# Kernel tuning notes

Measured on AMD Instinct MI355X. Metric: run time of the kernel, lower is better.

## Reference

```python
import jax, jax.numpy as jnp
import numpy as np

NUM_HEADS = 32
HEAD_DIM = 128
NUM_KV_HEADS = 8
SCALE = 0.08838834764831845  # 1/sqrt(128)
T = 2048          # total packed tokens (total_q == total_k in delta branch)
N_SAL = 512       # number of salient rows
NUM_SEQS = 4
EPS = 1e-8
NEG = -1e30


def setup_inputs() -> dict:
    key = jax.random.key(0)
    ks = jax.random.split(key, 5)
    q = jax.random.normal(ks[0], (T, NUM_HEADS, HEAD_DIM), dtype=jnp.float32)
    k = jax.random.normal(ks[1], (T, NUM_KV_HEADS, HEAD_DIM), dtype=jnp.float32)
    v = jax.random.normal(ks[2], (N_SAL, NUM_KV_HEADS, HEAD_DIM), dtype=jnp.float32)
    v_cache = jax.random.normal(ks[3], (T, NUM_KV_HEADS, HEAD_DIM), dtype=jnp.float32)
    c_cache = jax.random.normal(ks[4], (T, NUM_HEADS * HEAD_DIM), dtype=jnp.float32)
    # unique, sorted salient row indices (torch index_copy requires well-defined scatter)
    idx_salient_row = (jnp.arange(N_SAL, dtype=jnp.int64) * (T // N_SAL))
    # 4 equal packed sequences
    cu_seqlens = jnp.array([0, 512, 1024, 1536, 2048], dtype=jnp.int64)
    return {"q": q, "k": k, "v": v, "v_cache": v_cache, "c_cache": c_cache,
            "idx_salient_row": idx_salient_row, "cu_seqlens": cu_seqlens}


def _segment_ids(cu_seqlens, n):
    # seg[i] = which packed sequence row i belongs to (searchsorted right on bounds)
    return jnp.searchsorted(cu_seqlens[1:], jnp.arange(n), side="right")


def _sdpa(q_, k_, v_, seg_q_, seg_k_):
    # GQA: repeat_interleave kv heads to match query heads
    n_rep = q_.shape[1] // k_.shape[1]
    if n_rep > 1:
        k_ = jnp.repeat(k_, n_rep, axis=1)
        v_ = jnp.repeat(v_, n_rep, axis=1)
    scores = jnp.einsum("qhd,khd->hqk", q_, k_) * SCALE  # [H, nq, T]
    allow = (seg_q_[:, None] == seg_k_[None, :])          # [nq, T]
    scores = jnp.where(allow[None, :, :], scores, NEG)
    p = jax.nn.softmax(scores, axis=-1)
    return jnp.einsum("hqk,khd->qhd", p, v_)              # [nq, H, D]


def reference(q, k, v, v_cache, c_cache, idx_salient_row, cu_seqlens):
    total = q.shape[0]
    seg = _segment_ids(cu_seqlens, total)  # seg_q == seg_k (total_q == total_k)

    # delta KV-cache update at salient rows
    v_delta = v - v_cache[idx_salient_row]                      # [n_sal, Hkv, D]
    v_delta_sparse = jnp.zeros_like(k).at[idx_salient_row].set(v_delta)
    v_cache_new = v_cache.at[idx_salient_row].set(v)

    # salient-row full attention against updated cache
    o_salient = _sdpa(q[idx_salient_row], k, v_cache_new, seg[idx_salient_row], seg)
    # sparse delta attention for every row
    delta_c = _sdpa(q, k, v_delta_sparse, seg, seg)

    new_c_flat = c_cache + delta_c.reshape(total, -1)
    new_c_flat = new_c_flat.at[idx_salient_row].set(o_salient.reshape(o_salient.shape[0], -1))

    # cosine similarity between old and new context (early-exit signal)
    num = jnp.sum(c_cache * new_c_flat, axis=-1)
    den_c = jnp.sum(c_cache * c_cache, axis=-1)
    den_n = jnp.sum(new_c_flat * new_c_flat, axis=-1)
    cos_sim = num / (jnp.sqrt(den_c) * jnp.sqrt(den_n) + EPS)

    return new_c_flat.reshape(total, NUM_HEADS, HEAD_DIM), cos_sim
```

## Files before the change

kernel.cpp:

```cpp
#include <hip/hip_runtime.h>
#include <math.h>

#define NUM_HEADS 32
#define HEAD_DIM 128
#define NUM_KV_HEADS 8
#define SCALE 0.08838834764831845f
#define EPS 1e-8f
#define MAX_SEG 512
#define QT 32
#define BLK 512
#define SEGC_MAX 16
#define PB_STRIDE 520
#define TLD 130
#define CD (NUM_HEADS * HEAD_DIM)

typedef __bf16 bf16x8 __attribute__((ext_vector_type(8)));
typedef __bf16 bf16x4 __attribute__((ext_vector_type(4)));
typedef float  f32x4  __attribute__((ext_vector_type(4)));

__device__ __forceinline__ int lower_bound_i(const int* __restrict__ a, int n, int key) {
    int lo = 0, hi = n;
    while (lo < hi) { int mid = (lo + hi) >> 1; if (a[mid] < key) lo = mid + 1; else hi = mid; }
    return lo;
}
__device__ __forceinline__ int bsearch_eq(const int* __restrict__ a, int n, int key) {
    int lo = lower_bound_i(a, n, key);
    return (lo < n && a[lo] == key) ? lo : -1;
}

__device__ __forceinline__ bf16x8 cvt8(const float* p) {
    float4 f0 = *(const float4*)p;
    float4 f1 = *(const float4*)(p + 4);
    bf16x8 a;
    a[0]=(__bf16)f0.x; a[1]=(__bf16)f0.y; a[2]=(__bf16)f0.z; a[3]=(__bf16)f0.w;
    a[4]=(__bf16)f1.x; a[5]=(__bf16)f1.y; a[6]=(__bf16)f1.z; a[7]=(__bf16)f1.w;
    return a;
}

__device__ __forceinline__ void red16(float& xn, float& xc, float& xd) {
#pragma unroll
    for (int m = 1; m <= 8; m <<= 1) {
        xn += __shfl_xor(xn, m, 64);
        xc += __shfl_xor(xc, m, 64);
        xd += __shfl_xor(xd, m, 64);
    }
}

__global__ void prep(const float* __restrict__ k, const float* __restrict__ v,
                     const float* __restrict__ vc, const int* __restrict__ idx,
                     const int* __restrict__ cu,
                     __bf16* __restrict__ kb, __bf16* __restrict__ vnewT,
                     __bf16* __restrict__ vdScat, int* __restrict__ tinfo,
                     int* __restrict__ rowsal,
                     int T, int Tpad, int n_sal, int n_seq,
                     int nb_conv, int nb_vt) {
    __shared__ __bf16 tileN[64 * TLD];
    __shared__ __bf16 tileD[64 * TLD];
    __shared__ int sal_of[64];
    const int b = blockIdx.x;
    const int tid = threadIdx.x;

    if (b < nb_conv) {
        int i = b * 256 + tid;
        int n8 = T * NUM_KV_HEADS * HEAD_DIM / 8;
        if (i < n8) {
            const float4* s4 = (const float4*)(k + (size_t)i * 8);
            float4 a = s4[0], bb = s4[1];
            bf16x8 o;
            o[0]=(__bf16)a.x; o[1]=(__bf16)a.y; o[2]=(__bf16)a.z; o[3]=(__bf16)a.w;
            o[4]=(__bf16)bb.x; o[5]=(__bf16)bb.y; o[6]=(__bf16)bb.z; o[7]=(__bf16)bb.w;
            *(bf16x8*)(kb + (size_t)i * 8) = o;
        }
        return;
    }
    if (b < nb_conv + nb_vt * NUM_KV_HEADS) {
        const int bb = b - nb_conv;
        const int kv = bb / nb_vt;
        const int r0 = (bb % nb_vt) * 64;
        if (tid < 64) sal_of[tid] = bsearch_eq(idx, n_sal, r0 + tid);
        __syncthreads();
        for (int ii = tid; ii < 64 * 32; ii += 256) {
            int r = ii >> 5, c4 = ii & 31;
            int row = r0 + r;
            float4 fN = {0.f, 0.f, 0.f, 0.f};
            float4 fD = {0.f, 0.f, 0.f, 0.f};
            if (row < T) {
                int s2 = sal_of[r];
                if (s2 >= 0) {
                    float4 a  = *(const float4*)(v  + ((size_t)s2  * NUM_KV_HEADS + kv) * HEAD_DIM + c4 * 4);
                    float4 c  = *(const float4*)(vc + ((size_t)row * NUM_KV_HEADS + kv) * HEAD_DIM + c4 * 4);
                    fN = a;
                    fD.x = a.x - c.x; fD.y = a.y - c.y; fD.z = a.z - c.z; fD.w = a.w - c.w;
                } else {
                    fN = *(const float4*)(vc + ((size_t)row * NUM_KV_HEADS + kv) * HEAD_DIM + c4 * 4);
                }
            }
            __bf16* tn = &tileN[r * TLD + c4 * 4];
            tn[0] = (__bf16)fN.x; tn[1] = (__bf16)fN.y; tn[2] = (__bf16)fN.z; tn[3] = (__bf16)fN.w;
            __bf16* td = &tileD[r * TLD + c4 * 4];
            td[0] = (__bf16)fD.x; td[1] = (__bf16)fD.y; td[2] = (__bf16)fD.z; td[3] = (__bf16)fD.w;
        }
        __syncthreads();
        for (int ii = tid; ii < 128 * 8; ii += 256) {
            int d = ii >> 3, rg = ii & 7;
            int row_out = r0 + rg * 8;
            if (row_out < Tpad) {
                bf16x8 oN, oD;
#pragma unroll
                for (int j = 0; j < 8; j++) {
                    oN[j] = tileN[(rg * 8 + j) * TLD + d];
                    oD[j] = tileD[(rg * 8 + j) * TLD + d];
                }
                *(bf16x8*)(vnewT  + ((size_t)kv * HEAD_DIM + d) * Tpad + row_out) = oN;
                *(bf16x8*)(vdScat + ((size_t)kv * HEAD_DIM + d) * Tpad + row_out) = oD;
            }
        }
        return;
    }
    {
        for (int i = tid; i < T; i += 256) rowsal[i] = -1;
        __syncthreads();
        for (int s = tid; s < n_sal; s += 256) rowsal[idx[s]] = s;
        const int NT = T / QT;
        for (int t = tid; t < NT; t += 256) {
            const int r0 = t * QT;
            int a = 0, e = T;
            for (int s = 0; s < n_seq; s++) {
                int x = cu[s], y = cu[s + 1];
                if (r0 >= x && r0 < y) { a = x; e = y; }
            }
            tinfo[t * 4 + 0] = a;
            tinfo[t * 4 + 1] = e;
            tinfo[t * 4 + 2] = 0;
            tinfo[t * 4 + 3] = 0;
        }
    }
}


#define QK_TILE(ttc, FULLSEG) {                                                             \
    const int t_ = wave * 4 + (ttc);                                                        \
    if ((FULLSEG) || t_ < ntiles) {                                                         \
        int key_ = seg_start + t_ * 16 + lm;                                                \
        if (!(FULLSEG) && key_ >= seg_end) key_ = seg_end - 1;                              \
        const __bf16* kp_ = kb + ((size_t)key_ * NUM_KV_HEADS + kvh) * HEAD_DIM + quad * 8; \
        const bf16x8 bk0_ = *(const bf16x8*)(kp_);                                          \
        const bf16x8 bk1_ = *(const bf16x8*)(kp_ + 32);                                     \
        const bf16x8 bk2_ = *(const bf16x8*)(kp_ + 64);                                     \
        const bf16x8 bk3_ = *(const bf16x8*)(kp_ + 96);                                     \
        f32x4 a0_ = {0.f,0.f,0.f,0.f}, a1_ = {0.f,0.f,0.f,0.f};                             \
        a0_ = __builtin_amdgcn_mfma_f32_16x16x32_bf16(bk0_, aq00, a0_, 0, 0, 0);            \
        a1_ = __builtin_amdgcn_mfma_f32_16x16x32_bf16(bk0_, aq10, a1_, 0, 0, 0);            \
        a0_ = __builtin_amdgcn_mfma_f32_16x16x32_bf16(bk1_, aq01, a0_, 0, 0, 0);            \
        a1_ = __builtin_amdgcn_mfma_f32_16x16x32_bf16(bk1_, aq11, a1_, 0, 0, 0);            \
        a0_ = __builtin_amdgcn_mfma_f32_16x16x32_bf16(bk2_, aq02, a0_, 0, 0, 0);            \
        a1_ = __builtin_amdgcn_mfma_f32_16x16x32_bf16(bk2_, aq12, a1_, 0, 0, 0);            \
        a0_ = __builtin_amdgcn_mfma_f32_16x16x32_bf16(bk3_, aq03, a0_, 0, 0, 0);            \
        a1_ = __builtin_amdgcn_mfma_f32_16x16x32_bf16(bk3_, aq13, a1_, 0, 0, 0);            \
        bf16x4 pk0_, pk1_;                                                                  \
        _Pragma("unroll")                                                                   \
        for (int r_ = 0; r_ < 4; r_++) {                                                    \
            const int kl_ = t_ * 16 + quad * 4 + r_;                                        \
            const bool ok_ = (FULLSEG) || (kl_ < seg_len);                                  \
            float e0_ = ok_ ? __expf(a0_[r_] * SCALE) : 0.f;                                \
            float e1_ = ok_ ? __expf(a1_[r_] * SCALE) : 0.f;                                \
            ps0 += e0_; ps1 += e1_;                                                         \
            pk0_[r_] = (__bf16)e0_; pk1_[r_] = (__bf16)e1_;                                 \
        }                                                                                   \
        *(bf16x4*)&Pb[lm * PB_STRIDE + t_ * 16 + quad * 4] = pk0_;                          \
        *(bf16x4*)&Pb[(16 + lm) * PB_STRIDE + t_ * 16 + quad * 4] = pk1_;                   \
    } }

#define PV_BODY(cc) {                                                                       \
    const bf16x8 a0_ = *(const bf16x8*)(pb0 + (cc) * 32);                                   \
    const bf16x8 a1_ = *(const bf16x8*)(pb1 + (cc) * 32);                                   \
    const bf16x8 bF_ = *(const bf16x8*)(vF  + (cc) * 32);                                   \
    const bf16x8 bD_ = *(const bf16x8*)(vD  + (cc) * 32);                                   \
    accF0 = __builtin_amdgcn_mfma_f32_16x16x32_bf16(a0_, bF_, accF0, 0, 0, 0);              \
    accF1 = __builtin_amdgcn_mfma_f32_16x16x32_bf16(a1_, bF_, accF1, 0, 0, 0);              \
    accD0 = __builtin_amdgcn_mfma_f32_16x16x32_bf16(a0_, bD_, accD0, 0, 0, 0);              \
    accD1 = __builtin_amdgcn_mfma_f32_16x16x32_bf16(a1_, bD_, accD1, 0, 0, 0); }

__global__ __launch_bounds__(BLK, 6)
void attn_mfma(const float* __restrict__ q, const __bf16* __restrict__ kb,
               const __bf16* __restrict__ vnewT, const __bf16* __restrict__ vdScat,
               const float* __restrict__ c_cache, const int* __restrict__ tinfo,
               const int* __restrict__ rowsal,
               float* __restrict__ out_c, float* __restrict__ cospart, int Tpad) {
    const int bid  = blockIdx.x;
    const int kvh  = bid & 7;
    const int rem  = bid >> 3;
    const int h    = kvh * 4 + (rem & 3);
    const int qt   = rem >> 2;
    const int qrow0 = qt * QT;
    const int tid   = threadIdx.x;
    const int wave  = tid >> 6;
    const int lane  = tid & 63;
    const int lm    = lane & 15;
    const int quad  = lane >> 4;

    __shared__ __align__(16) __bf16 Pb[QT * PB_STRIDE];
    __shared__ float wred[8 * QT];
    __shared__ float linv[QT];
    __shared__ int   salrow[QT];
    __shared__ float cp[8 * 3 * QT];

    const int4 ti = *(const int4*)(tinfo + qt * 4);
    const int seg_start = ti.x, seg_end = ti.y;
    const int seg_len = seg_end - seg_start;
    const int ntiles = (seg_len + 15) >> 4;
    const int SEGC   = (seg_len + 31) >> 5;
    const int dim = wave * 16 + lm;

    if (tid < QT) salrow[tid] = rowsal[qrow0 + tid];
    if (ntiles * 16 < SEGC * 32) {
        for (int ii = tid; ii < QT * 16; ii += BLK) {
            int row = ii >> 4, col = ntiles * 16 + (ii & 15);
            Pb[row * PB_STRIDE + col] = (__bf16)0.f;
        }
    }

    bf16x8 aq00, aq01, aq02, aq03, aq10, aq11, aq12, aq13;
    {
        const float* qp0 = q + ((size_t)(qrow0 + lm) * NUM_HEADS + h) * HEAD_DIM + quad * 8;
        const float* qp1 = q + ((size_t)(qrow0 + 16 + lm) * NUM_HEADS + h) * HEAD_DIM + quad * 8;
        aq00 = cvt8(qp0);      aq01 = cvt8(qp0 + 32); aq02 = cvt8(qp0 + 64); aq03 = cvt8(qp0 + 96);
        aq10 = cvt8(qp1);      aq11 = cvt8(qp1 + 32); aq12 = cvt8(qp1 + 64); aq13 = cvt8(qp1 + 96);
    }

    float ps0 = 0.f, ps1 = 0.f;
    if (seg_len == MAX_SEG) {
        QK_TILE(0, 1) QK_TILE(1, 1) QK_TILE(2, 1) QK_TILE(3, 1)
    } else {
        QK_TILE(0, 0) QK_TILE(1, 0) QK_TILE(2, 0) QK_TILE(3, 0)
    }
#pragma unroll
    for (int m = 16; m <= 32; m <<= 1) {
        ps0 += __shfl_xor(ps0, m, 64);
        ps1 += __shfl_xor(ps1, m, 64);
    }
    if (quad == 0) {
        wred[wave * QT + lm]      = ps0;
        wred[wave * QT + 16 + lm] = ps1;
    }
    __syncthreads();
    if (tid < QT) {
        float s = 0.f;
#pragma unroll
        for (int w = 0; w < 8; w++) s += wred[w * QT + tid];
        linv[tid] = 1.f / s;
    }

    const float* cbase = c_cache + (size_t)qrow0 * CD + h * HEAD_DIM + dim;
    float cold[2][4];
#pragma unroll
    for (int rt = 0; rt < 2; rt++)
#pragma unroll
        for (int r = 0; r < 4; r++)
            cold[rt][r] = cbase[(size_t)(rt * 16 + quad * 4 + r) * CD];

    __builtin_amdgcn_s_setprio(1);
    f32x4 accF0 = {0.f,0.f,0.f,0.f}, accF1 = {0.f,0.f,0.f,0.f};
    f32x4 accD0 = {0.f,0.f,0.f,0.f}, accD1 = {0.f,0.f,0.f,0.f};
    const __bf16* vF = vnewT  + ((size_t)kvh * HEAD_DIM + dim) * Tpad + seg_start + quad * 8;
    const __bf16* vD = vdScat + ((size_t)kvh * HEAD_DIM + dim) * Tpad + seg_start + quad * 8;
    const __bf16* pb0 = &Pb[lm * PB_STRIDE + quad * 8];
    const __bf16* pb1 = &Pb[(16 + lm) * PB_STRIDE + quad * 8];
    if (SEGC == SEGC_MAX) {
#pragma unroll
        for (int cc = 0; cc < SEGC_MAX; cc++) PV_BODY(cc)
    } else {
        for (int cc = 0; cc < SEGC; cc++) PV_BODY(cc)
    }
    __builtin_amdgcn_s_setprio(0);
    __syncthreads();

    float* obase = out_c + (size_t)qrow0 * CD + h * HEAD_DIM + dim;
#pragma unroll
    for (int rt = 0; rt < 2; rt++) {
#pragma unroll
        for (int r = 0; r < 4; r++) {
            const int row = rt * 16 + quad * 4 + r;
            const float c_old = cold[rt][r];
            const float li = linv[row];
            const float aF = (rt == 0) ? accF0[r] : accF1[r];
            const float aD = (rt == 0) ? accD0[r] : accD1[r];
            const float o = (salrow[row] >= 0) ? aF * li : c_old + aD * li;
            obase[(size_t)row * CD] = o;
            float xn = o * c_old, xc = c_old * c_old, xd = o * o;
            red16(xn, xc, xd);
            if (lm == 0) {
                cp[(wave * 3 + 0) * QT + row] = xn;
                cp[(wave * 3 + 1) * QT + row] = xc;
                cp[(wave * 3 + 2) * QT + row] = xd;
            }
        }
    }
    __syncthreads();
    for (int ii = tid; ii < 3 * QT; ii += BLK) {
        int c = ii >> 5, row = ii & 31;
        float s = 0.f;
#pragma unroll
        for (int w = 0; w < 8; w++) s += cp[(w * 3 + c) * QT + row];
        cospart[((size_t)(qrow0 + row) * 3 + c) * NUM_HEADS + h] = s;
    }
}

__global__ void cos_finalize(const float* __restrict__ cospart, float* __restrict__ out_cos, int T) {
    const int lane = threadIdx.x & 63;
    const int row  = blockIdx.x * 4 + (threadIdx.x >> 6);
    if (row >= T) return;
    const float* p = cospart + (size_t)row * (NUM_HEADS * 3);
    float a = p[lane];
    float b = (lane < 32) ? p[64 + lane] : 0.f;
#pragma unroll
    for (int m = 1; m <= 16; m <<= 1) {
        a += __shfl_xor(a, m, 64);
        b += __shfl_xor(b, m, 64);
    }
    float den_c = __shfl(a, 32, 64);
    if (lane == 0) out_cos[row] = a / (sqrtf(den_c) * sqrtf(b) + EPS);
}

extern "C" void kernel_launch(void* const* d_in, const int* in_sizes, int n_in,
                              void* d_out, int out_size, void* d_ws, size_t ws_size,
                              hipStream_t stream) {
    const float* q       = (const float*)d_in[0];
    const float* k       = (const float*)d_in[1];
    const float* v       = (const float*)d_in[2];
    const float* v_cache = (const float*)d_in[3];
    const float* c_cache = (const float*)d_in[4];
    const int*   idx     = (const int*)d_in[5];
    const int*   cu      = (const int*)d_in[6];

    const int T     = in_sizes[0] / CD;
    const int n_sal = in_sizes[5];
    const int n_seq = in_sizes[6] - 1;
    const int Tpad  = T + 32;
    const int NT    = T / QT;

    float* out_c   = (float*)d_out;
    float* out_cos = out_c + (size_t)T * CD;

    char* wsp = (char*)d_ws;
    size_t off = 0;
    __bf16* kb = (__bf16*)(wsp + off);
    off += (((size_t)T * NUM_KV_HEADS * HEAD_DIM * 2) + 255) & ~(size_t)255;
    __bf16* vnewT = (__bf16*)(wsp + off);
    off += (((size_t)NUM_KV_HEADS * HEAD_DIM * Tpad * 2) + 255) & ~(size_t)255;
    __bf16* vdScat = (__bf16*)(wsp + off);
    off += (((size_t)NUM_KV_HEADS * HEAD_DIM * Tpad * 2) + 255) & ~(size_t)255;
    float* cospart = (float*)(wsp + off);
    off += ((size_t)T * NUM_HEADS * 3 * 4 + 255) & ~(size_t)255;
    int* tinfo = (int*)(wsp + off);
    off += ((size_t)NT * 4 * 4 + 255) & ~(size_t)255;
    int* rowsal = (int*)(wsp + off);
    off += ((size_t)T * 4 + 255) & ~(size_t)255;
    (void)ws_size;

    const int nb_conv = (T * NUM_KV_HEADS * HEAD_DIM / 8 + 255) / 256;
    const int nb_vt   = (Tpad + 63) / 64;
    const int nb_tot  = nb_conv + nb_vt * NUM_KV_HEADS + 1;

    prep<<<nb_tot, 256, 0, stream>>>(k, v, v_cache, idx, cu, kb, vnewT, vdScat,
                                     tinfo, rowsal, T, Tpad, n_sal, n_seq,
                                     nb_conv, nb_vt);

    attn_mfma<<<NT * NUM_HEADS, BLK, 0, stream>>>(q, kb, vnewT, vdScat, c_cache,
                                                  tinfo, rowsal, out_c, cospart, Tpad);

    cos_finalize<<<(T + 3) / 4, 256, 0, stream>>>(cospart, out_cos, T);
}
```

Before: 233.6 us.

## Software-pipeline K and V loads with register double-buffering in attention kernel

```diff
diff --git a/kernel.cpp b/kernel.cpp
--- a/kernel.cpp
+++ b/kernel.cpp
@@ -17,6 +17,8 @@
 typedef __bf16 bf16x8 __attribute__((ext_vector_type(8)));
 typedef __bf16 bf16x4 __attribute__((ext_vector_type(4)));
 typedef float  f32x4  __attribute__((ext_vector_type(4)));
+
+#define MFMA16(a, b, c) __builtin_amdgcn_mfma_f32_16x16x32_bf16((a), (b), (c), 0, 0, 0)
 
 __device__ __forceinline__ int lower_bound_i(const int* __restrict__ a, int n, int key) {
     int lo = 0, hi = n;
@@ -138,30 +140,26 @@
 }
 
 
-#define QK_TILE(ttc, FULLSEG) {                                                             \
+#define QK_TILE_GEN(ttc) {                                                                  \
     const int t_ = wave * 4 + (ttc);                                                        \
-    if ((FULLSEG) || t_ < ntiles) {                                                         \
+    if (t_ < ntiles) {                                                                      \
         int key_ = seg_start + t_ * 16 + lm;                                                \
-        if (!(FULLSEG) && key_ >= seg_end) key_ = seg_end - 1;                              \
+        if (key_ >= seg_end) key_ = seg_end - 1;                                            \
         const __bf16* kp_ = kb + ((size_t)key_ * NUM_KV_HEADS + kvh) * HEAD_DIM + quad * 8; \
         const bf16x8 bk0_ = *(const bf16x8*)(kp_);                                          \
         const bf16x8 bk1_ = *(const bf16x8*)(kp_ + 32);                                     \
         const bf16x8 bk2_ = *(const bf16x8*)(kp_ + 64);                                     \
         const bf16x8 bk3_ = *(const bf16x8*)(kp_ + 96);                                     \
         f32x4 a0_ = {0.f,0.f,0.f,0.f}, a1_ = {0.f,0.f,0.f,0.f};                             \
-        a0_ = __builtin_amdgcn_mfma_f32_16x16x32_bf16(bk0_, aq00, a0_, 0, 0, 0);            \
-        a1_ = __builtin_amdgcn_mfma_f32_16x16x32_bf16(bk0_, aq10, a1_, 0, 0, 0);            \
-        a0_ = __builtin_amdgcn_mfma_f32_16x16x32_bf16(bk1_, aq01, a0_, 0, 0, 0);            \
-        a1_ = __builtin_amdgcn_mfma_f32_16x16x32_bf16(bk1_, aq11, a1_, 0, 0, 0);            \
-        a0_ = __builtin_amdgcn_mfma_f32_16x16x32_bf16(bk2_, aq02, a0_, 0, 0, 0);            \
-        a1_ = __builtin_amdgcn_mfma_f32_16x16x32_bf16(bk2_, aq12, a1_, 0, 0, 0);            \
-        a0_ = __builtin_amdgcn_mfma_f32_16x16x32_bf16(bk3_, aq03, a0_, 0, 0, 0);            \
-        a1_ = __builtin_amdgcn_mfma_f32_16x16x32_bf16(bk3_, aq13, a1_, 0, 0, 0);            \
+        a0_ = MFMA16(bk0_, aq00, a0_);  a1_ = MFMA16(bk0_, aq10, a1_);                      \
+        a0_ = MFMA16(bk1_, aq01, a0_);  a1_ = MFMA16(bk1_, aq11, a1_);                      \
+        a0_ = MFMA16(bk2_, aq02, a0_);  a1_ = MFMA16(bk2_, aq12, a1_);                      \
+        a0_ = MFMA16(bk3_, aq03, a0_);  a1_ = MFMA16(bk3_, aq13, a1_);                      \
         bf16x4 pk0_, pk1_;                                                                  \
         _Pragma("unroll")                                                                   \
         for (int r_ = 0; r_ < 4; r_++) {                                                    \
             const int kl_ = t_ * 16 + quad * 4 + r_;                                        \
-            const bool ok_ = (FULLSEG) || (kl_ < seg_len);                                  \
+            const bool ok_ = (kl_ < seg_len);                                               \
             float e0_ = ok_ ? __expf(a0_[r_] * SCALE) : 0.f;                                \
             float e1_ = ok_ ? __expf(a1_[r_] * SCALE) : 0.f;                                \
             ps0 += e0_; ps1 += e1_;                                                         \
@@ -171,17 +169,7 @@
         *(bf16x4*)&Pb[(16 + lm) * PB_STRIDE + t_ * 16 + quad * 4] = pk1_;                   \
     } }
 
-#define PV_BODY(cc) {                                                                       \
-    const bf16x8 a0_ = *(const bf16x8*)(pb0 + (cc) * 32);                                   \
-    const bf16x8 a1_ = *(const bf16x8*)(pb1 + (cc) * 32);                                   \
-    const bf16x8 bF_ = *(const bf16x8*)(vF  + (cc) * 32);                                   \
-    const bf16x8 bD_ = *(const bf16x8*)(vD  + (cc) * 32);                                   \
-    accF0 = __builtin_amdgcn_mfma_f32_16x16x32_bf16(a0_, bF_, accF0, 0, 0, 0);              \
-    accF1 = __builtin_amdgcn_mfma_f32_16x16x32_bf16(a1_, bF_, accF1, 0, 0, 0);              \
-    accD0 = __builtin_amdgcn_mfma_f32_16x16x32_bf16(a0_, bD_, accD0, 0, 0, 0);              \
-    accD1 = __builtin_amdgcn_mfma_f32_16x16x32_bf16(a1_, bD_, accD1, 0, 0, 0); }
-
-__global__ __launch_bounds__(BLK, 6)
+__global__ __launch_bounds__(BLK, 4)
 void attn_mfma(const float* __restrict__ q, const __bf16* __restrict__ kb,
                const __bf16* __restrict__ vnewT, const __bf16* __restrict__ vdScat,
                const float* __restrict__ c_cache, const int* __restrict__ tinfo,
@@ -228,11 +216,53 @@
         aq10 = cvt8(qp1);      aq11 = cvt8(qp1 + 32); aq12 = cvt8(qp1 + 64); aq13 = cvt8(qp1 + 96);
     }
 
+    const float* cbase = c_cache + (size_t)qrow0 * CD + h * HEAD_DIM + dim;
+    float cold[2][4];
+#pragma unroll
+    for (int rt = 0; rt < 2; rt++)
+#pragma unroll
+        for (int r = 0; r < 4; r++)
+            cold[rt][r] = cbase[(size_t)(rt * 16 + quad * 4 + r) * CD];
+
     float ps0 = 0.f, ps1 = 0.f;
     if (seg_len == MAX_SEG) {
-        QK_TILE(0, 1) QK_TILE(1, 1) QK_TILE(2, 1) QK_TILE(3, 1)
+        const size_t krow = (size_t)NUM_KV_HEADS * HEAD_DIM;
+        const __bf16* kp = kb + (size_t)(seg_start + wave * 64 + lm) * krow
+                              + (size_t)kvh * HEAD_DIM + quad * 8;
+        bf16x8 kk[2][4];
+        kk[0][0] = *(const bf16x8*)(kp);
+        kk[0][1] = *(const bf16x8*)(kp + 32);
+        kk[0][2] = *(const bf16x8*)(kp + 64);
+        kk[0][3] = *(const bf16x8*)(kp + 96);
+#pragma unroll
+        for (int tt = 0; tt < 4; tt++) {
+            const int cur = tt & 1, nxt = cur ^ 1;
+            if (tt < 3) {
+                const __bf16* kn = kp + (size_t)(tt + 1) * 16 * krow;
+                kk[nxt][0] = *(const bf16x8*)(kn);
+                kk[nxt][1] = *(const bf16x8*)(kn + 32);
+                kk[nxt][2] = *(const bf16x8*)(kn + 64);
+                kk[nxt][3] = *(const bf16x8*)(kn + 96);
+            }
+            f32x4 a0_ = {0.f,0.f,0.f,0.f}, a1_ = {0.f,0.f,0.f,0.f};
+            a0_ = MFMA16(kk[cur][0], aq00, a0_);  a1_ = MFMA16(kk[cur][0], aq10, a1_);
+            a0_ = MFMA16(kk[cur][1], aq01, a0_);  a1_ = MFMA16(kk[cur][1], aq11, a1_);
+            a0_ = MFMA16(kk[cur][2], aq02, a0_);  a1_ = MFMA16(kk[cur][2], aq12, a1_);
+            a0_ = MFMA16(kk[cur][3], aq03, a0_);  a1_ = MFMA16(kk[cur][3], aq13, a1_);
+            const int t_ = wave * 4 + tt;
+            bf16x4 pk0_, pk1_;
+#pragma unroll
+            for (int r_ = 0; r_ < 4; r_++) {
+                float e0_ = __expf(a0_[r_] * SCALE);
+                float e1_ = __expf(a1_[r_] * SCALE);
+                ps0 += e0_; ps1 += e1_;
+                pk0_[r_] = (__bf16)e0_; pk1_[r_] = (__bf16)e1_;
+            }
+            *(bf16x4*)&Pb[lm * PB_STRIDE + t_ * 16 + quad * 4] = pk0_;
+            *(bf16x4*)&Pb[(16 + lm) * PB_STRIDE + t_ * 16 + quad * 4] = pk1_;
+        }
     } else {
-        QK_TILE(0, 0) QK_TILE(1, 0) QK_TILE(2, 0) QK_TILE(3, 0)
+        QK_TILE_GEN(0) QK_TILE_GEN(1) QK_TILE_GEN(2) QK_TILE_GEN(3)
     }
 #pragma unroll
     for (int m = 16; m <= 32; m <<= 1) {
@@ -243,34 +273,56 @@
         wred[wave * QT + lm]      = ps0;
         wred[wave * QT + 16 + lm] = ps1;
     }
-    __syncthreads();
-    if (tid < QT) {
-        float s = 0.f;
-#pragma unroll
-        for (int w = 0; w < 8; w++) s += wred[w * QT + tid];
-        linv[tid] = 1.f / s;
-    }
-
-    const float* cbase = c_cache + (size_t)qrow0 * CD + h * HEAD_DIM + dim;
-    float cold[2][4];
-#pragma unroll
-    for (int rt = 0; rt < 2; rt++)
-#pragma unroll
-        for (int r = 0; r < 4; r++)
-            cold[rt][r] = cbase[(size_t)(rt * 16 + quad * 4 + r) * CD];
-
-    __builtin_amdgcn_s_setprio(1);
-    f32x4 accF0 = {0.f,0.f,0.f,0.f}, accF1 = {0.f,0.f,0.f,0.f};
-    f32x4 accD0 = {0.f,0.f,0.f,0.f}, accD1 = {0.f,0.f,0.f,0.f};
+
     const __bf16* vF = vnewT  + ((size_t)kvh * HEAD_DIM + dim) * Tpad + seg_start + quad * 8;
     const __bf16* vD = vdScat + ((size_t)kvh * HEAD_DIM + dim) * Tpad + seg_start + quad * 8;
     const __bf16* pb0 = &Pb[lm * PB_STRIDE + quad * 8];
     const __bf16* pb1 = &Pb[(16 + lm) * PB_STRIDE + quad * 8];
+    bf16x8 fv[2], dv[2];
+    fv[0] = *(const bf16x8*)vF;
+    dv[0] = *(const bf16x8*)vD;
+
+    __syncthreads();
+    if (tid < QT) {
+        float s = 0.f;
+#pragma unroll
+        for (int w = 0; w < 8; w++) s += wred[w * QT + tid];
+        linv[tid] = 1.f / s;
+    }
+
+    __builtin_amdgcn_s_setprio(1);
+    f32x4 accF0 = {0.f,0.f,0.f,0.f}, accF1 = {0.f,0.f,0.f,0.f};
+    f32x4 accD0 = {0.f,0.f,0.f,0.f}, accD1 = {0.f,0.f,0.f,0.f};
     if (SEGC == SEGC_MAX) {
-#pragma unroll
-        for (int cc = 0; cc < SEGC_MAX; cc++) PV_BODY(cc)
+        bf16x8 a0c = *(const bf16x8*)(pb0);
+        bf16x8 a1c = *(const bf16x8*)(pb1);
+#pragma unroll
+        for (int cc = 0; cc < SEGC_MAX; cc++) {
+            const int cur = cc & 1, nxt = cur ^ 1;
+            bf16x8 a0n, a1n;
+            if (cc < SEGC_MAX - 1) {
+                fv[nxt] = *(const bf16x8*)(vF + (cc + 1) * 32);
+                dv[nxt] = *(const bf16x8*)(vD + (cc + 1) * 32);
+                a0n = *(const bf16x8*)(pb0 + (cc + 1) * 32);
+                a1n = *(const bf16x8*)(pb1 + (cc + 1) * 32);
+            }
+            accF0 = MFMA16(a0c, fv[cur], accF0);
+            accF1 = MFMA16(a1c, fv[cur], accF1);
+            accD0 = MFMA16(a0c, dv[cur], accD0);
+            accD1 = MFMA16(a1c, dv[cur], accD1);
+            if (cc < SEGC_MAX - 1) { a0c = a0n; a1c = a1n; }
+        }
     } else {
-        for (int cc = 0; cc < SEGC; cc++) PV_BODY(cc)
+        for (int cc = 0; cc < SEGC; cc++) {
+            const bf16x8 bF_ = *(const bf16x8*)(vF + cc * 32);
+            const bf16x8 bD_ = *(const bf16x8*)(vD + cc * 32);
+            const bf16x8 a0_ = *(const bf16x8*)(pb0 + cc * 32);
+            const bf16x8 a1_ = *(const bf16x8*)(pb1 + cc * 32);
+            accF0 = MFMA16(a0_, bF_, accF0);
+            accF1 = MFMA16(a1_, bF_, accF1);
+            accD0 = MFMA16(a0_, bD_, accD0);
+            accD1 = MFMA16(a1_, bD_, accD1);
+        }
     }
     __builtin_amdgcn_s_setprio(0);
     __syncthreads();
```

After: 230.6 us. Within noise of the previous version (-1.3%).

## Halve query tile to 16 rows with 256-thread blocks and rebalance wave work

Applied to the files above, without the earlier changes.

```diff
diff --git a/kernel.cpp b/kernel.cpp
--- a/kernel.cpp
+++ b/kernel.cpp
@@ -7,8 +7,8 @@
 #define SCALE 0.08838834764831845f
 #define EPS 1e-8f
 #define MAX_SEG 512
-#define QT 32
-#define BLK 512
+#define QT 16
+#define BLK 256
 #define SEGC_MAX 16
 #define PB_STRIDE 520
 #define TLD 130
@@ -17,6 +17,8 @@
 typedef __bf16 bf16x8 __attribute__((ext_vector_type(8)));
 typedef __bf16 bf16x4 __attribute__((ext_vector_type(4)));
 typedef float  f32x4  __attribute__((ext_vector_type(4)));
+
+#define MFMA16(a, b, c) __builtin_amdgcn_mfma_f32_16x16x32_bf16((a), (b), (c), 0, 0, 0)
 
 __device__ __forceinline__ int lower_bound_i(const int* __restrict__ a, int n, int key) {
     int lo = 0, hi = n;
@@ -138,50 +140,7 @@
 }
 
 
-#define QK_TILE(ttc, FULLSEG) {                                                             \
-    const int t_ = wave * 4 + (ttc);                                                        \
-    if ((FULLSEG) || t_ < ntiles) {                                                         \
-        int key_ = seg_start + t_ * 16 + lm;                                                \
-        if (!(FULLSEG) && key_ >= seg_end) key_ = seg_end - 1;                              \
-        const __bf16* kp_ = kb + ((size_t)key_ * NUM_KV_HEADS + kvh) * HEAD_DIM + quad * 8; \
-        const bf16x8 bk0_ = *(const bf16x8*)(kp_);                                          \
-        const bf16x8 bk1_ = *(const bf16x8*)(kp_ + 32);                                     \
-        const bf16x8 bk2_ = *(const bf16x8*)(kp_ + 64);                                     \
-        const bf16x8 bk3_ = *(const bf16x8*)(kp_ + 96);                                     \
-        f32x4 a0_ = {0.f,0.f,0.f,0.f}, a1_ = {0.f,0.f,0.f,0.f};                             \
-        a0_ = __builtin_amdgcn_mfma_f32_16x16x32_bf16(bk0_, aq00, a0_, 0, 0, 0);            \
-        a1_ = __builtin_amdgcn_mfma_f32_16x16x32_bf16(bk0_, aq10, a1_, 0, 0, 0);            \
-        a0_ = __builtin_amdgcn_mfma_f32_16x16x32_bf16(bk1_, aq01, a0_, 0, 0, 0);            \
-        a1_ = __builtin_amdgcn_mfma_f32_16x16x32_bf16(bk1_, aq11, a1_, 0, 0, 0);            \
-        a0_ = __builtin_amdgcn_mfma_f32_16x16x32_bf16(bk2_, aq02, a0_, 0, 0, 0);            \
-        a1_ = __builtin_amdgcn_mfma_f32_16x16x32_bf16(bk2_, aq12, a1_, 0, 0, 0);            \
-        a0_ = __builtin_amdgcn_mfma_f32_16x16x32_bf16(bk3_, aq03, a0_, 0, 0, 0);            \
-        a1_ = __builtin_amdgcn_mfma_f32_16x16x32_bf16(bk3_, aq13, a1_, 0, 0, 0);            \
-        bf16x4 pk0_, pk1_;                                                                  \
-        _Pragma("unroll")                                                                   \
-        for (int r_ = 0; r_ < 4; r_++) {                                                    \
-            const int kl_ = t_ * 16 + quad * 4 + r_;                                        \
-            const bool ok_ = (FULLSEG) || (kl_ < seg_len);                                  \
-            float e0_ = ok_ ? __expf(a0_[r_] * SCALE) : 0.f;                                \
-            float e1_ = ok_ ? __expf(a1_[r_] * SCALE) : 0.f;                                \
-            ps0 += e0_; ps1 += e1_;                                                         \
-            pk0_[r_] = (__bf16)e0_; pk1_[r_] = (__bf16)e1_;                                 \
-        }                                                                                   \
-        *(bf16x4*)&Pb[lm * PB_STRIDE + t_ * 16 + quad * 4] = pk0_;                          \
-        *(bf16x4*)&Pb[(16 + lm) * PB_STRIDE + t_ * 16 + quad * 4] = pk1_;                   \
-    } }
-
-#define PV_BODY(cc) {                                                                       \
-    const bf16x8 a0_ = *(const bf16x8*)(pb0 + (cc) * 32);                                   \
-    const bf16x8 a1_ = *(const bf16x8*)(pb1 + (cc) * 32);                                   \
-    const bf16x8 bF_ = *(const bf16x8*)(vF  + (cc) * 32);                                   \
-    const bf16x8 bD_ = *(const bf16x8*)(vD  + (cc) * 32);                                   \
-    accF0 = __builtin_amdgcn_mfma_f32_16x16x32_bf16(a0_, bF_, accF0, 0, 0, 0);              \
-    accF1 = __builtin_amdgcn_mfma_f32_16x16x32_bf16(a1_, bF_, accF1, 0, 0, 0);              \
-    accD0 = __builtin_amdgcn_mfma_f32_16x16x32_bf16(a0_, bD_, accD0, 0, 0, 0);              \
-    accD1 = __builtin_amdgcn_mfma_f32_16x16x32_bf16(a1_, bD_, accD1, 0, 0, 0); }
-
-__global__ __launch_bounds__(BLK, 6)
+__global__ __launch_bounds__(BLK, 8)
 void attn_mfma(const float* __restrict__ q, const __bf16* __restrict__ kb,
                const __bf16* __restrict__ vnewT, const __bf16* __restrict__ vdScat,
                const float* __restrict__ c_cache, const int* __restrict__ tinfo,
@@ -200,7 +159,7 @@
     const int quad  = lane >> 4;
 
     __shared__ __align__(16) __bf16 Pb[QT * PB_STRIDE];
-    __shared__ float wred[8 * QT];
+    __shared__ float wred[4 * QT];
     __shared__ float linv[QT];
     __shared__ int   salrow[QT];
     __shared__ float cp[8 * 3 * QT];
@@ -210,7 +169,6 @@
     const int seg_len = seg_end - seg_start;
     const int ntiles = (seg_len + 15) >> 4;
     const int SEGC   = (seg_len + 31) >> 5;
-    const int dim = wave * 16 + lm;
 
     if (tid < QT) salrow[tid] = rowsal[qrow0 + tid];
     if (ntiles * 16 < SEGC * 32) {
@@ -220,88 +178,143 @@
         }
     }
 
-    bf16x8 aq00, aq01, aq02, aq03, aq10, aq11, aq12, aq13;
-    {
-        const float* qp0 = q + ((size_t)(qrow0 + lm) * NUM_HEADS + h) * HEAD_DIM + quad * 8;
-        const float* qp1 = q + ((size_t)(qrow0 + 16 + lm) * NUM_HEADS + h) * HEAD_DIM + quad * 8;
-        aq00 = cvt8(qp0);      aq01 = cvt8(qp0 + 32); aq02 = cvt8(qp0 + 64); aq03 = cvt8(qp0 + 96);
-        aq10 = cvt8(qp1);      aq11 = cvt8(qp1 + 32); aq12 = cvt8(qp1 + 64); aq13 = cvt8(qp1 + 96);
-    }
-
-    float ps0 = 0.f, ps1 = 0.f;
+    const float* qp = q + ((size_t)(qrow0 + lm) * NUM_HEADS + h) * HEAD_DIM + quad * 8;
+    const bf16x8 aqA = cvt8(qp);
+    const bf16x8 aqB = cvt8(qp + 32);
+    const bf16x8 aqC = cvt8(qp + 64);
+    const bf16x8 aqD = cvt8(qp + 96);
+
+    float ps = 0.f;
     if (seg_len == MAX_SEG) {
-        QK_TILE(0, 1) QK_TILE(1, 1) QK_TILE(2, 1) QK_TILE(3, 1)
+        const size_t krow = (size_t)NUM_KV_HEADS * HEAD_DIM;
+        const __bf16* kp = kb + (size_t)(seg_start + wave * 128 + lm) * krow
+                              + (size_t)kvh * HEAD_DIM + quad * 8;
+#pragma unroll
+        for (int tt = 0; tt < 8; tt++) {
+            const __bf16* kt = kp + (size_t)tt * 16 * krow;
+            const bf16x8 bk0 = *(const bf16x8*)(kt);
+            const bf16x8 bk1 = *(const bf16x8*)(kt + 32);
+            const bf16x8 bk2 = *(const bf16x8*)(kt + 64);
+            const bf16x8 bk3 = *(const bf16x8*)(kt + 96);
+            f32x4 a_ = {0.f,0.f,0.f,0.f};
+            a_ = MFMA16(bk0, aqA, a_);
+            a_ = MFMA16(bk1, aqB, a_);
+            a_ = MFMA16(bk2, aqC, a_);
+            a_ = MFMA16(bk3, aqD, a_);
+            const int t_ = wave * 8 + tt;
+            bf16x4 pk;
+#pragma unroll
+            for (int r = 0; r < 4; r++) {
+                float e = __expf(a_[r] * SCALE);
+                ps += e;
+                pk[r] = (__bf16)e;
+            }
+            *(bf16x4*)&Pb[lm * PB_STRIDE + t_ * 16 + quad * 4] = pk;
+        }
     } else {
-        QK_TILE(0, 0) QK_TILE(1, 0) QK_TILE(2, 0) QK_TILE(3, 0)
-    }
-#pragma unroll
-    for (int m = 16; m <= 32; m <<= 1) {
-        ps0 += __shfl_xor(ps0, m, 64);
-        ps1 += __shfl_xor(ps1, m, 64);
-    }
-    if (quad == 0) {
-        wred[wave * QT + lm]      = ps0;
-        wred[wave * QT + 16 + lm] = ps1;
-    }
+        for (int tt = 0; tt < 8; tt++) {
+            const int t_ = wave * 8 + tt;
+            if (t_ < ntiles) {
+                int key = seg_start + t_ * 16 + lm;
+                if (key >= seg_end) key = seg_end - 1;
+                const __bf16* kt = kb + ((size_t)key * NUM_KV_HEADS + kvh) * HEAD_DIM + quad * 8;
+                const bf16x8 bk0 = *(const bf16x8*)(kt);
+                const bf16x8 bk1 = *(const bf16x8*)(kt + 32);
+                const bf16x8 bk2 = *(const bf16x8*)(kt + 64);
+                const bf16x8 bk3 = *(const bf16x8*)(kt + 96);
+                f32x4 a_ = {0.f,0.f,0.f,0.f};
+                a_ = MFMA16(bk0, aqA, a_);
+                a_ = MFMA16(bk1, aqB, a_);
+                a_ = MFMA16(bk2, aqC, a_);
+                a_ = MFMA16(bk3, aqD, a_);
+                bf16x4 pk;
+#pragma unroll
+                for (int r = 0; r < 4; r++) {
+                    const int kl = t_ * 16 + quad * 4 + r;
+                    float e = (kl < seg_len) ? __expf(a_[r] * SCALE) : 0.f;
+                    ps += e;
+                    pk[r] = (__bf16)e;
+                }
+                *(bf16x4*)&Pb[lm * PB_STRIDE + t_ * 16 + quad * 4] = pk;
+            }
+        }
+    }
+#pragma unroll
+    for (int m = 16; m <= 32; m <<= 1) ps += __shfl_xor(ps, m, 64);
+    if (quad == 0) wred[wave * QT + lm] = ps;
+
     __syncthreads();
     if (tid < QT) {
         float s = 0.f;
 #pragma unroll
-        for (int w = 0; w < 8; w++) s += wred[w * QT + tid];
+        for (int w = 0; w < 4; w++) s += wred[w * QT + tid];
         linv[tid] = 1.f / s;
     }
 
-    const float* cbase = c_cache + (size_t)qrow0 * CD + h * HEAD_DIM + dim;
-    float cold[2][4];
-#pragma unroll
-    for (int rt = 0; rt < 2; rt++)
-#pragma unroll
-        for (int r = 0; r < 4; r++)
-            cold[rt][r] = cbase[(size_t)(rt * 16 + quad * 4 + r) * CD];
+    const int gdim = wave * 32 + lm;
+    const __bf16* vF0 = vnewT  + ((size_t)kvh * HEAD_DIM + gdim) * Tpad + seg_start + quad * 8;
+    const __bf16* vD0 = vdScat + ((size_t)kvh * HEAD_DIM + gdim) * Tpad + seg_start + quad * 8;
+    const __bf16* vF1 = vF0 + (size_t)16 * Tpad;
+    const __bf16* vD1 = vD0 + (size_t)16 * Tpad;
+    const __bf16* pb0 = &Pb[lm * PB_STRIDE + quad * 8];
 
     __builtin_amdgcn_s_setprio(1);
     f32x4 accF0 = {0.f,0.f,0.f,0.f}, accF1 = {0.f,0.f,0.f,0.f};
     f32x4 accD0 = {0.f,0.f,0.f,0.f}, accD1 = {0.f,0.f,0.f,0.f};
-    const __bf16* vF = vnewT  + ((size_t)kvh * HEAD_DIM + dim) * Tpad + seg_start + quad * 8;
-    const __bf16* vD = vdScat + ((size_t)kvh * HEAD_DIM + dim) * Tpad + seg_start + quad * 8;
-    const __bf16* pb0 = &Pb[lm * PB_STRIDE + quad * 8];
-    const __bf16* pb1 = &Pb[(16 + lm) * PB_STRIDE + quad * 8];
+#define PVB(cc) {                                                   \
+        const bf16x8 a0_ = *(const bf16x8*)(pb0 + (cc) * 32);       \
+        const bf16x8 f0_ = *(const bf16x8*)(vF0 + (cc) * 32);       \
+        const bf16x8 f1_ = *(const bf16x8*)(vF1 + (cc) * 32);       \
+        const bf16x8 d0_ = *(const bf16x8*)(vD0 + (cc) * 32);       \
+        const bf16x8 d1_ = *(const bf16x8*)(vD1 + (cc) * 32);       \
+        accF0 = MFMA16(a0_, f0_, accF0);                            \
+        accF1 = MFMA16(a0_, f1_, accF1);                            \
+        accD0 = MFMA16(a0_, d0_, accD0);                            \
+        accD1 = MFMA16(a0_, d1_, accD1); }
     if (SEGC == SEGC_MAX) {
 #pragma unroll
-        for (int cc = 0; cc < SEGC_MAX; cc++) PV_BODY(cc)
+        for (int cc = 0; cc < SEGC_MAX; cc++) PVB(cc)
     } else {
-        for (int cc = 0; cc < SEGC; cc++) PV_BODY(cc)
-    }
+        for (int cc = 0; cc < SEGC; cc++) PVB(cc)
+    }
+#undef PVB
     __builtin_amdgcn_s_setprio(0);
     __syncthreads();
 
-    float* obase = out_c + (size_t)qrow0 * CD + h * HEAD_DIM + dim;
-#pragma unroll
-    for (int rt = 0; rt < 2; rt++) {
+    const float* cb0 = c_cache + (size_t)qrow0 * CD + h * HEAD_DIM + gdim;
+    float* ob0 = out_c + (size_t)qrow0 * CD + h * HEAD_DIM + gdim;
+#pragma unroll
+    for (int g = 0; g < 2; g++) {
+        const f32x4 aF = g ? accF1 : accF0;
+        const f32x4 aD = g ? accD1 : accD0;
+        const float* cb = cb0 + g * 16;
+        float* ob = ob0 + g * 16;
+        float cold[4];
+#pragma unroll
+        for (int r = 0; r < 4; r++) cold[r] = cb[(size_t)(quad * 4 + r) * CD];
 #pragma unroll
         for (int r = 0; r < 4; r++) {
-            const int row = rt * 16 + quad * 4 + r;
-            const float c_old = cold[rt][r];
+            const int row = quad * 4 + r;
+            const float c_old = cold[r];
             const float li = linv[row];
-            const float aF = (rt == 0) ? accF0[r] : accF1[r];
-            const float aD = (rt == 0) ? accD0[r] : accD1[r];
-            const float o = (salrow[row] >= 0) ? aF * li : c_old + aD * li;
-            obase[(size_t)row * CD] = o;
+            const float o = (salrow[row] >= 0) ? aF[r] * li : c_old + aD[r] * li;
+            ob[(size_t)row * CD] = o;
             float xn = o * c_old, xc = c_old * c_old, xd = o * o;
             red16(xn, xc, xd);
             if (lm == 0) {
-                cp[(wave * 3 + 0) * QT + row] = xn;
-                cp[(wave * 3 + 1) * QT + row] = xc;
-                cp[(wave * 3 + 2) * QT + row] = xd;
+                const int slot = wave * 2 + g;
+                cp[(slot * 3 + 0) * QT + row] = xn;
+                cp[(slot * 3 + 1) * QT + row] = xc;
+                cp[(slot * 3 + 2) * QT + row] = xd;
             }
         }
     }
     __syncthreads();
     for (int ii = tid; ii < 3 * QT; ii += BLK) {
-        int c = ii >> 5, row = ii & 31;
+        int c = ii >> 4, row = ii & 15;
         float s = 0.f;
 #pragma unroll
-        for (int w = 0; w < 8; w++) s += cp[(w * 3 + c) * QT + row];
+        for (int k = 0; k < 8; k++) s += cp[(k * 3 + c) * QT + row];
         cospart[((size_t)(qrow0 + row) * 3 + c) * NUM_HEADS + h] = s;
     }
 }
```

Result: slower. 275.9 us (+18.1%).
